# Optimization experiments

Measured on AMD Instinct MI355X. Metric: run time of the kernel, lower is better.

The kernel has to match this reference:

```python
import jax, jax.numpy as jnp
import numpy as np

N_NODES, N_EDGES, F_IN = 8192, 32768, 16
N_SUB, N_GRAPH = 512, 32
EDGE_DIM, HID = 5, 128
DIMS = [(16, 32), (32, 64), (64, 64)]  # (M_in, M_out) per NNConv layer


def _segment_mean(x, seg, n):
    s = jax.ops.segment_sum(x, seg, num_segments=n)
    c = jax.ops.segment_sum(jnp.ones((x.shape[0], 1), x.dtype), seg, num_segments=n)
    return s / jnp.maximum(c, 1.0)


def _nnconv(x, src, dst, eattr, W1, b1, W2, b2, root, bias):
    # edge MLP -> per-edge weight matrix theta: [E, M_in, M_out]
    h = jax.nn.relu(eattr @ W1 + b1)
    theta = (h @ W2 + b2).reshape(-1, x.shape[1], root.shape[1])
    msg = jnp.einsum('ei,eio->eo', x[src], theta)          # gather + per-edge matvec
    agg = jax.ops.segment_sum(msg, dst, num_segments=x.shape[0])  # scatter-add (aggr='add')
    return agg + x @ root + bias


def setup_inputs() -> dict:
    key = jax.random.key(0)
    ks = jax.random.split(key, 32)
    inp = {}
    inp['x'] = jax.random.normal(ks[0], (N_NODES, F_IN), jnp.float32)
    inp['edge_index'] = jax.random.randint(ks[1], (2, N_EDGES), 0, N_NODES)
    inp['edge_attr'] = jax.random.uniform(ks[2], (N_EDGES, EDGE_DIM), jnp.float32)
    inp['node_to_subgraph'] = jnp.sort(jax.random.randint(ks[3], (N_NODES,), 0, N_SUB))
    inp['subgraph_to_graph'] = jnp.sort(jax.random.randint(ks[4], (N_SUB,), 0, N_GRAPH))
    i = 5
    for l, (ci, co) in enumerate(DIMS):
        inp[f'W1_{l}'] = jax.random.normal(ks[i], (EDGE_DIM, HID), jnp.float32) * 0.1
        inp[f'b1_{l}'] = jnp.zeros((HID,), jnp.float32)
        inp[f'W2_{l}'] = jax.random.normal(ks[i + 1], (HID, ci * co), jnp.float32) * 0.05
        inp[f'b2_{l}'] = jnp.zeros((ci * co,), jnp.float32)
        inp[f'root_{l}'] = jax.random.normal(ks[i + 2], (ci, co), jnp.float32) * 0.1
        inp[f'bias_{l}'] = jnp.zeros((co,), jnp.float32)
        i += 3
    inp['fc1_w'] = jax.random.normal(ks[i], (64, 32), jnp.float32) * 0.1
    inp['fc1_b'] = jnp.zeros((32,), jnp.float32)
    inp['fc2_w'] = jax.random.normal(ks[i + 1], (32, 16), jnp.float32) * 0.1
    inp['fc2_b'] = jnp.zeros((16,), jnp.float32)
    inp['fc3_w'] = jax.random.normal(ks[i + 2], (16, 1), jnp.float32) * 0.1
    inp['fc3_b'] = jnp.zeros((1,), jnp.float32)
    return inp


def reference(x, edge_index, edge_attr, node_to_subgraph, subgraph_to_graph,
              W1_0, b1_0, W2_0, b2_0, root_0, bias_0,
              W1_1, b1_1, W2_1, b2_1, root_1, bias_1,
              W1_2, b1_2, W2_2, b2_2, root_2, bias_2,
              fc1_w, fc1_b, fc2_w, fc2_b, fc3_w, fc3_b):
    src, dst = edge_index[0], edge_index[1]
    layers = [(W1_0, b1_0, W2_0, b2_0, root_0, bias_0),
              (W1_1, b1_1, W2_1, b2_1, root_1, bias_1),
              (W1_2, b1_2, W2_2, b2_2, root_2, bias_2)]
    h = x
    for (W1, b1, W2, b2, root, bias) in layers:
        h = jax.nn.elu(_nnconv(h, src, dst, edge_attr, W1, b1, W2, b2, root, bias))
    h = _segment_mean(h, node_to_subgraph, N_SUB)      # global_mean_pool over subgraphs
    h = _segment_mean(h, subgraph_to_graph, N_GRAPH)   # global_mean_pool over graphs
    h = jax.nn.elu(h @ fc1_w + fc1_b)
    h = jax.nn.elu(h @ fc2_w + fc2_b)
    return (h @ fc3_w + fc3_b).reshape(-1)
```

## Files before the change

kernel.cpp:

```cpp
#include <hip/hip_runtime.h>

#define E_EDGES 32768
#define NN 8192
#define HID 128
#define KS 4

typedef _Float16 half8 __attribute__((ext_vector_type(8)));
typedef _Float16 half4 __attribute__((ext_vector_type(4)));
typedef float f32x4 __attribute__((ext_vector_type(4)));

__global__ void hist_k(const int* __restrict__ dst, int* __restrict__ hist) {
  int e = blockIdx.x * 256 + threadIdx.x;
  if (e < E_EDGES) atomicAdd(&hist[dst[e]], 1);
}

__global__ void scan_k(const int* __restrict__ hist, int* __restrict__ roff, int* __restrict__ cursor) {
  __shared__ int wsum[16];
  int t = threadIdx.x;
  int lane = t & 63, wv = t >> 6;
  int base = t * 8;
  int loc[8]; int s = 0;
#pragma unroll
  for (int j = 0; j < 8; ++j) { loc[j] = s; s += hist[base + j]; }
  int inc = s;
#pragma unroll
  for (int off = 1; off < 64; off <<= 1) {
    int u = __shfl_up(inc, off, 64);
    if (lane >= off) inc += u;
  }
  if (lane == 63) wsum[wv] = inc;
  __syncthreads();
  if (t < 64) {
    int u = (t < 16) ? wsum[t] : 0;
#pragma unroll
    for (int off = 1; off < 16; off <<= 1) {
      int x = __shfl_up(u, off, 64);
      if (lane >= off) u += x;
    }
    if (t < 16) wsum[t] = u;
  }
  __syncthreads();
  int excl = (wv ? wsum[wv - 1] : 0) + inc - s;
#pragma unroll
  for (int j = 0; j < 8; ++j) { int v = excl + loc[j]; roff[base + j] = v; cursor[base + j] = v; }
  if (t == 1023) roff[NN] = wsum[15];
}

__global__ void scatter_k(const int* __restrict__ dst, int* __restrict__ cursor, int* __restrict__ eidx) {
  int e = blockIdx.x * 256 + threadIdx.x;
  if (e < E_EDGES) { int p = atomicAdd(&cursor[dst[e]], 1); eidx[p] = e; }
}

template <int CI, int CO>
__device__ inline void prep8(int h8, const float* __restrict__ W2,
                             const float* __restrict__ b2, _Float16* __restrict__ out) {
  constexpr int Kmain = 128 * CI;
  constexpr int FC = CO / 16;
  int lane = h8 & 63;
  int quad = lane >> 4, l15 = lane & 15;
  int rest = h8 >> 6;
  int fc = rest & (FC - 1);
  int c = rest / FC;
  int k0 = c * 32 + quad * 8;
  int n = fc * 16 + l15;
  half8 r;
#pragma unroll
  for (int j = 0; j < 8; ++j) {
    int k = k0 + j;
    float v = 0.f;
    if (k < Kmain) v = W2[(size_t)k * CO + n];
    else if (k < Kmain + CI) v = b2[(k - Kmain) * CO + n];
    r[j] = (_Float16)v;
  }
  *(half8*)(out + (size_t)h8 * 8) = r;
}

__global__ void prep_zero_k(const float* __restrict__ W2_0, const float* __restrict__ b2_0, _Float16* __restrict__ o0,
                            const float* __restrict__ W2_1, const float* __restrict__ b2_1, _Float16* __restrict__ o1,
                            const float* __restrict__ W2_2, const float* __restrict__ b2_2, _Float16* __restrict__ o2,
                            int4* __restrict__ hist4, float4* __restrict__ pools4) {
  constexpr int H0 = 2176 * 32 / 8;
  constexpr int H1 = 4224 * 64 / 8;
  constexpr int H2 = 8320 * 64 / 8;
  constexpr int HT = H0 + H1 + H2;
  constexpr int ZH = NN / 4;
  constexpr int ZP = (512 * 64 + 512) / 4;
  int tid = blockIdx.x * 256 + threadIdx.x;
  if (tid < H0) prep8<16, 32>(tid, W2_0, b2_0, o0);
  else if (tid < H0 + H1) prep8<32, 64>(tid - H0, W2_1, b2_1, o1);
  else if (tid < HT) prep8<64, 64>(tid - H0 - H1, W2_2, b2_2, o2);
  else if (tid < HT + ZH) hist4[tid - HT] = int4{0, 0, 0, 0};
  else if (tid < HT + ZH + ZP) pools4[tid - HT - ZH] = float4{0.f, 0.f, 0.f, 0.f};
}

__device__ inline half8 pack8(float4 a, float4 b) {
  half8 r;
  r[0] = (_Float16)a.x; r[1] = (_Float16)a.y; r[2] = (_Float16)a.z; r[3] = (_Float16)a.w;
  r[4] = (_Float16)b.x; r[5] = (_Float16)b.y; r[6] = (_Float16)b.z; r[7] = (_Float16)b.w;
  return r;
}

__device__ __forceinline__ void gload_lds16(const _Float16* g, _Float16* l) {
  __builtin_amdgcn_global_load_lds(
      (__attribute__((address_space(1))) void*)(size_t)(const void*)g,
      (__attribute__((address_space(3))) void*)(size_t)(void*)l, 16, 0, 0);
}

template <int CI, int CO>
__launch_bounds__(256, 2)
__global__ void msg_mfma_k(const float* __restrict__ xcur, const int* __restrict__ src,
                           const int* __restrict__ eidx,
                           const float* __restrict__ eattr, const float* __restrict__ W1,
                           const float* __restrict__ b1, const _Float16* __restrict__ Bsw,
                           float* __restrict__ msgbuf) {
  constexpr int ME = 256;
  constexpr int HSTR = 36;
  constexpr int FC = CO / 16;
  constexpr int NMAIN = CI / 4;
  constexpr int XPN = (CI == 64) ? 2 : 1;
  constexpr int RHALF = 4 * FC * 64 * 8;

  __shared__ _Float16 he_s[ME * HSTR];
  __shared__ float ea_s[ME * 5];
  __shared__ float W1s[5 * 32];
  __shared__ float b1s[32];
  __shared__ int src_s[ME];
  __shared__ _Float16 bls[2 * RHALF];

  int t = threadIdx.x;
  int e0 = blockIdx.x * ME;
  int y = blockIdx.y;
  int hbeg = y * 32;

  {
    int eg = eidx[e0 + t];
    src_s[t] = src[eg];
#pragma unroll
    for (int d = 0; d < 5; ++d) ea_s[t * 5 + d] = eattr[eg * 5 + d];
  }
  if (t < 5 * 32) W1s[t] = W1[(t >> 5) * HID + hbeg + (t & 31)];
  if (t < 32) b1s[t] = b1[hbeg + t];
  __syncthreads();

  for (int j = t; j < 32 * ME; j += 256) {
    int hl = j & 31, e = j >> 5;
    float v = b1s[hl];
#pragma unroll
    for (int d = 0; d < 5; ++d) v += ea_s[e * 5 + d] * W1s[d * 32 + hl];
    he_s[e * HSTR + hl] = (_Float16)fmaxf(v, 0.f);
  }
  __syncthreads();

  int lane = t & 63;
  int w = t >> 6;
  int quad = lane >> 4, l15 = lane & 15;
  int qsh = (quad >> 1) << 4;
  int Rg0 = y * NMAIN;
  int NR = NMAIN + ((y == 3) ? 1 : 0);

  half8 xp[4][XPN];
  int hoff[4];
#pragma unroll
  for (int fr = 0; fr < 4; ++fr) {
    int e = w * 64 + fr * 16 + l15;
    const float* xr = xcur + (size_t)src_s[e] * CI;
    int i0 = (CI == 16) ? ((quad & 1) * 8) : (quad * 8);
    float4 v0 = *(const float4*)(xr + i0);
    float4 v1 = *(const float4*)(xr + i0 + 4);
    xp[fr][0] = pack8(v0, v1);
    if constexpr (CI == 64) {
      float4 v2 = *(const float4*)(xr + i0 + 32);
      float4 v3 = *(const float4*)(xr + i0 + 36);
      xp[fr][1] = pack8(v2, v3);
    }
    hoff[fr] = e * HSTR;
  }

  f32x4 acc[4][FC];
#pragma unroll
  for (int fr = 0; fr < 4; ++fr)
#pragma unroll
    for (int fc = 0; fc < FC; ++fc)
#pragma unroll
      for (int r = 0; r < 4; ++r) acc[fr][fc][r] = 0.f;

  auto stageR = [&](int rg, int buf) {
    const _Float16* gb = Bsw + (size_t)rg * RHALF + w * (FC * 512);
    _Float16* lb = bls + buf * RHALF + w * (FC * 512);
#pragma unroll
    for (int i = 0; i < FC; ++i)
      gload_lds16(gb + i * 512 + lane * 8, lb + i * 512);
  };

  stageR(Rg0, 0);
  stageR(Rg0 + 1, 1);

  for (int r = 0; r < NR; ++r) {
    if (r + 1 < NR) {
      if constexpr (FC == 4) asm volatile("s_waitcnt vmcnt(4)" ::: "memory");
      else                   asm volatile("s_waitcnt vmcnt(2)" ::: "memory");
    } else {
      asm volatile("s_waitcnt vmcnt(0)" ::: "memory");
    }
    __builtin_amdgcn_s_barrier();

    const _Float16* bp = bls + (r & 1) * RHALF;
    int c0 = (Rg0 + r) * 4;

    if (r < NMAIN) {
      unsigned int hp2[4];
      half4 hp4[4];
      if constexpr (CI == 64) {
        int oh = (c0 >> 1) - hbeg;
#pragma unroll
        for (int fr = 0; fr < 4; ++fr) hp2[fr] = *(const unsigned int*)(he_s + hoff[fr] + oh);
      } else if constexpr (CI == 32) {
        int oh = c0 - hbeg;
#pragma unroll
        for (int fr = 0; fr < 4; ++fr) hp4[fr] = *(const half4*)(he_s + hoff[fr] + oh);
      }
#pragma unroll
      for (int cr = 0; cr < 4; ++cr) {
        int c = c0 + cr;
        half8 a[4];
#pragma unroll
        for (int fr = 0; fr < 4; ++fr) {
          if constexpr (CI == 64) {
            unsigned short hb = (unsigned short)((cr >= 2) ? (hp2[fr] >> 16) : hp2[fr]);
            _Float16 hv = __builtin_bit_cast(_Float16, hb);
            a[fr] = xp[fr][cr & 1] * hv;
          } else if constexpr (CI == 32) {
            a[fr] = xp[fr][0] * hp4[fr][cr];
          } else {
            unsigned int hw = *(const unsigned int*)(he_s + hoff[fr] + (2 * c - hbeg));
            _Float16 hv = __builtin_bit_cast(_Float16, (unsigned short)(hw >> qsh));
            a[fr] = xp[fr][0] * hv;
          }
        }
#pragma unroll
        for (int fc = 0; fc < FC; ++fc) {
          half8 bf = *(const half8*)&bp[((cr * FC + fc) * 64 + lane) * 8];
#pragma unroll
          for (int fr = 0; fr < 4; ++fr)
            acc[fr][fc] = __builtin_amdgcn_mfma_f32_16x16x32_f16(a[fr], bf, acc[fr][fc], 0, 0, 0);
        }
      }
    } else {
#pragma unroll
      for (int cr = 0; cr < 4; ++cr) {
        half8 a[4];
#pragma unroll
        for (int fr = 0; fr < 4; ++fr) a[fr] = xp[fr][(CI == 64) ? (cr & 1) : 0];
#pragma unroll
        for (int fc = 0; fc < FC; ++fc) {
          half8 bf = *(const half8*)&bp[((cr * FC + fc) * 64 + lane) * 8];
#pragma unroll
          for (int fr = 0; fr < 4; ++fr)
            acc[fr][fc] = __builtin_amdgcn_mfma_f32_16x16x32_f16(a[fr], bf, acc[fr][fc], 0, 0, 0);
        }
      }
    }

    asm volatile("s_waitcnt lgkmcnt(0)" ::: "memory");
    __builtin_amdgcn_s_barrier();
    if (r + 2 < NR) stageR(Rg0 + r + 2, r & 1);
  }

#pragma unroll
  for (int fr = 0; fr < 4; ++fr)
#pragma unroll
    for (int fc = 0; fc < FC; ++fc)
#pragma unroll
      for (int r = 0; r < 4; ++r) {
        int el = w * 64 + fr * 16 + quad * 4 + r;
        int o = fc * 16 + l15;
        msgbuf[((size_t)(e0 + el) * KS + y) * CO + o] = acc[fr][fc][r];
      }
}

template <int CI, int CO, bool POOL>
__global__ void gather_elu_k(const float* __restrict__ xcur, const float* __restrict__ root,
                             const float* __restrict__ bias, const float* __restrict__ msgbuf,
                             const int* __restrict__ roff,
                             float* __restrict__ xnext, const int* __restrict__ n2s,
                             float* __restrict__ ssum, float* __restrict__ scnt) {
  constexpr int OV = CO / 4;
  constexpr int NB = 256 / OV;
  __shared__ float xs[NB * CI];
  int t = threadIdx.x;
  int n0 = blockIdx.x * NB;
  for (int j = t; j < NB * CI; j += 256) xs[j] = xcur[n0 * CI + j];
  __syncthreads();
  int nl = t / OV, o4 = t & (OV - 1);
  int n = n0 + nl;
  float4 a = ((const float4*)bias)[o4];
  const float4* root4 = (const float4*)root;
#pragma unroll
  for (int i = 0; i < CI; ++i) {
    float xv = xs[nl * CI + i];
    float4 rv = root4[i * OV + o4];
    a.x += xv * rv.x; a.y += xv * rv.y; a.z += xv * rv.z; a.w += xv * rv.w;
  }
  int j1 = roff[n + 1];
  const float4* mb4 = (const float4*)msgbuf;
  for (int p = roff[n]; p < j1; ++p) {
#pragma unroll
    for (int s = 0; s < KS; ++s) {
      float4 m = mb4[((size_t)p * KS + s) * OV + o4];
      a.x += m.x; a.y += m.y; a.z += m.z; a.w += m.w;
    }
  }
  float4 v;
  v.x = a.x > 0.f ? a.x : expm1f(a.x);
  v.y = a.y > 0.f ? a.y : expm1f(a.y);
  v.z = a.z > 0.f ? a.z : expm1f(a.z);
  v.w = a.w > 0.f ? a.w : expm1f(a.w);
  if constexpr (POOL) {
    int s = n2s[n];
    float* sb = &ssum[(s << 6) + o4 * 4];
    atomicAdd(sb + 0, v.x); atomicAdd(sb + 1, v.y);
    atomicAdd(sb + 2, v.z); atomicAdd(sb + 3, v.w);
    if (o4 == 0) atomicAdd(&scnt[s], 1.f);
  } else {
    ((float4*)xnext)[(size_t)n * OV + o4] = v;
  }
}

__global__ void pg_head_k(const float* __restrict__ ssum, const float* __restrict__ scnt,
                          const int* __restrict__ s2g,
                          const float* __restrict__ w1, const float* __restrict__ b1,
                          const float* __restrict__ w2, const float* __restrict__ b2,
                          const float* __restrict__ w3, const float* __restrict__ b3,
                          float* __restrict__ out) {
  int g = blockIdx.x;
  int t = threadIdx.x;
  __shared__ int s2s[512];
  __shared__ float hm[64], h1[32], h2[16];
  for (int i = t; i < 512; i += 64) s2s[i] = s2g[i];
  __syncthreads();
  float acc = 0.f, cnt = 0.f;
  for (int s = 0; s < 512; ++s) {
    if (s2s[s] == g) {
      acc += ssum[(s << 6) + t] / fmaxf(scnt[s], 1.f);
      cnt += 1.f;
    }
  }
  hm[t] = acc / fmaxf(cnt, 1.f);
  __syncthreads();
  if (t < 32) {
    float a = b1[t];
    for (int i = 0; i < 64; ++i) a += hm[i] * w1[i * 32 + t];
    h1[t] = a > 0.f ? a : expm1f(a);
  }
  __syncthreads();
  if (t < 16) {
    float a = b2[t];
    for (int i = 0; i < 32; ++i) a += h1[i] * w2[i * 16 + t];
    h2[t] = a > 0.f ? a : expm1f(a);
  }
  __syncthreads();
  if (t == 0) {
    float a = b3[0];
    for (int i = 0; i < 16; ++i) a += h2[i] * w3[i];
    out[g] = a;
  }
}

extern "C" void kernel_launch(void* const* d_in, const int* in_sizes, int n_in,
                              void* d_out, int out_size, void* d_ws, size_t ws_size,
                              hipStream_t stream) {
  (void)in_sizes; (void)n_in; (void)out_size; (void)ws_size;
  const float* x0 = (const float*)d_in[0];
  const int* ei = (const int*)d_in[1];
  const float* ea = (const float*)d_in[2];
  const int* n2s = (const int*)d_in[3];
  const int* s2g = (const int*)d_in[4];
  const float* W1_[3] = {(const float*)d_in[5], (const float*)d_in[11], (const float*)d_in[17]};
  const float* b1_[3] = {(const float*)d_in[6], (const float*)d_in[12], (const float*)d_in[18]};
  const float* W2_[3] = {(const float*)d_in[7], (const float*)d_in[13], (const float*)d_in[19]};
  const float* b2_[3] = {(const float*)d_in[8], (const float*)d_in[14], (const float*)d_in[20]};
  const float* rt_[3] = {(const float*)d_in[9], (const float*)d_in[15], (const float*)d_in[21]};
  const float* bs_[3] = {(const float*)d_in[10], (const float*)d_in[16], (const float*)d_in[22]};
  const float* fc1w = (const float*)d_in[23]; const float* fc1b = (const float*)d_in[24];
  const float* fc2w = (const float*)d_in[25]; const float* fc2b = (const float*)d_in[26];
  const float* fc3w = (const float*)d_in[27]; const float* fc3b = (const float*)d_in[28];
  float* out = (float*)d_out;

  const int* srcp = ei;
  const int* dstp = ei + E_EDGES;

  char* wsb = (char*)d_ws;
  size_t off = 0;
  auto alloc = [&](size_t bytes) {
    void* p = wsb + off;
    off += (bytes + 255) & ~(size_t)255;
    return p;
  };
  _Float16* Bsw0 = (_Float16*)alloc((size_t)2176 * 32 * 2);
  _Float16* Bsw1 = (_Float16*)alloc((size_t)4224 * 64 * 2);
  _Float16* Bsw2 = (_Float16*)alloc((size_t)8320 * 64 * 2);
  float* msgbuf = (float*)alloc((size_t)KS * E_EDGES * 64 * 4);
  float* x1 = (float*)alloc((size_t)NN * 32 * 4);
  float* x2 = (float*)alloc((size_t)NN * 64 * 4);
  int* hist = (int*)alloc((size_t)NN * 4);
  int* roff = (int*)alloc((size_t)(NN + 1) * 4);
  int* cursor = (int*)alloc((size_t)NN * 4);
  int* eidx = (int*)alloc((size_t)E_EDGES * 4);
  const int npool = 512 * 64 + 512;
  float* pools = (float*)alloc((size_t)npool * 4);
  float* ssum = pools;
  float* scnt = pools + 512 * 64;

  const int nprep = 109056 + 2048 + 8320;
  prep_zero_k<<<(nprep + 255) / 256, 256, 0, stream>>>(
      W2_[0], b2_[0], Bsw0, W2_[1], b2_[1], Bsw1, W2_[2], b2_[2], Bsw2,
      (int4*)hist, (float4*)pools);
  hist_k<<<E_EDGES / 256, 256, 0, stream>>>(dstp, hist);
  scan_k<<<1, 1024, 0, stream>>>(hist, roff, cursor);
  scatter_k<<<E_EDGES / 256, 256, 0, stream>>>(dstp, cursor, eidx);

  dim3 mg(E_EDGES / 256, KS);
  msg_mfma_k<16, 32><<<mg, 256, 0, stream>>>(x0, srcp, eidx, ea, W1_[0], b1_[0], Bsw0, msgbuf);
  gather_elu_k<16, 32, false><<<NN / 32, 256, 0, stream>>>(x0, rt_[0], bs_[0], msgbuf, roff, x1, nullptr, nullptr, nullptr);
  msg_mfma_k<32, 64><<<mg, 256, 0, stream>>>(x1, srcp, eidx, ea, W1_[1], b1_[1], Bsw1, msgbuf);
  gather_elu_k<32, 64, false><<<NN / 16, 256, 0, stream>>>(x1, rt_[1], bs_[1], msgbuf, roff, x2, nullptr, nullptr, nullptr);
  msg_mfma_k<64, 64><<<mg, 256, 0, stream>>>(x2, srcp, eidx, ea, W1_[2], b1_[2], Bsw2, msgbuf);
  gather_elu_k<64, 64, true><<<NN / 16, 256, 0, stream>>>(x2, rt_[2], bs_[2], msgbuf, roff, nullptr, n2s, ssum, scnt);

  pg_head_k<<<32, 64, 0, stream>>>(ssum, scnt, s2g, fc1w, fc1b, fc2w, fc2b, fc3w, fc3b, out);
}
```

Baseline: 278.6 us.

## Halve edge tile and split message-kernel warps across output columns and edges

The per-edge message MFMA kernel now processes 128 edges per block instead of 256, which doubles the grid. Its four warps are split between output-column fragments and edge groups instead of each warp covering 64 edges across all output columns. This gives each warp fewer accumulators and one B fragment load per row step, aiming at better occupancy and more blocks to fill the GPU. In exchange, each block stages the weight tiles for half as many edges, and source features are gathered redundantly by warps that share edges.

```diff
diff --git a/kernel.cpp b/kernel.cpp
--- a/kernel.cpp
+++ b/kernel.cpp
@@ -113,9 +113,12 @@
                            const float* __restrict__ eattr, const float* __restrict__ W1,
                            const float* __restrict__ b1, const _Float16* __restrict__ Bsw,
                            float* __restrict__ msgbuf) {
-  constexpr int ME = 256;
+  constexpr int ME = 128;
   constexpr int HSTR = 36;
   constexpr int FC = CO / 16;
+  constexpr int WN = (FC == 4) ? 4 : 2;
+  constexpr int WE = 4 / WN;
+  constexpr int FR = (ME / 16) / WE;
   constexpr int NMAIN = CI / 4;
   constexpr int XPN = (CI == 64) ? 2 : 1;
   constexpr int RHALF = 4 * FC * 64 * 8;
@@ -132,7 +135,7 @@
   int y = blockIdx.y;
   int hbeg = y * 32;
 
-  {
+  if (t < ME) {
     int eg = eidx[e0 + t];
     src_s[t] = src[eg];
 #pragma unroll
@@ -153,16 +156,17 @@
 
   int lane = t & 63;
   int w = t >> 6;
+  int wn = w % WN, we = w / WN;
   int quad = lane >> 4, l15 = lane & 15;
   int qsh = (quad >> 1) << 4;
   int Rg0 = y * NMAIN;
   int NR = NMAIN + ((y == 3) ? 1 : 0);
 
-  half8 xp[4][XPN];
-  int hoff[4];
-#pragma unroll
-  for (int fr = 0; fr < 4; ++fr) {
-    int e = w * 64 + fr * 16 + l15;
+  half8 xp[FR][XPN];
+  int hoff[FR];
+#pragma unroll
+  for (int fr = 0; fr < FR; ++fr) {
+    int e = we * (FR * 16) + fr * 16 + l15;
     const float* xr = xcur + (size_t)src_s[e] * CI;
     int i0 = (CI == 16) ? ((quad & 1) * 8) : (quad * 8);
     float4 v0 = *(const float4*)(xr + i0);
@@ -176,13 +180,11 @@
     hoff[fr] = e * HSTR;
   }
 
-  f32x4 acc[4][FC];
-#pragma unroll
-  for (int fr = 0; fr < 4; ++fr)
-#pragma unroll
-    for (int fc = 0; fc < FC; ++fc)
-#pragma unroll
-      for (int r = 0; r < 4; ++r) acc[fr][fc][r] = 0.f;
+  f32x4 acc[FR];
+#pragma unroll
+  for (int fr = 0; fr < FR; ++fr)
+#pragma unroll
+    for (int r = 0; r < 4; ++r) acc[fr][r] = 0.f;
 
   auto stageR = [&](int rg, int buf) {
     const _Float16* gb = Bsw + (size_t)rg * RHALF + w * (FC * 512);
@@ -208,55 +210,46 @@
     int c0 = (Rg0 + r) * 4;
 
     if (r < NMAIN) {
-      unsigned int hp2[4];
-      half4 hp4[4];
+      unsigned int hp2[FR];
+      half4 hp4[FR];
       if constexpr (CI == 64) {
         int oh = (c0 >> 1) - hbeg;
 #pragma unroll
-        for (int fr = 0; fr < 4; ++fr) hp2[fr] = *(const unsigned int*)(he_s + hoff[fr] + oh);
+        for (int fr = 0; fr < FR; ++fr) hp2[fr] = *(const unsigned int*)(he_s + hoff[fr] + oh);
       } else if constexpr (CI == 32) {
         int oh = c0 - hbeg;
 #pragma unroll
-        for (int fr = 0; fr < 4; ++fr) hp4[fr] = *(const half4*)(he_s + hoff[fr] + oh);
+        for (int fr = 0; fr < FR; ++fr) hp4[fr] = *(const half4*)(he_s + hoff[fr] + oh);
       }
 #pragma unroll
       for (int cr = 0; cr < 4; ++cr) {
         int c = c0 + cr;
-        half8 a[4];
-#pragma unroll
-        for (int fr = 0; fr < 4; ++fr) {
+        half8 bf = *(const half8*)&bp[((cr * FC + wn) * 64 + lane) * 8];
+#pragma unroll
+        for (int fr = 0; fr < FR; ++fr) {
+          half8 a;
           if constexpr (CI == 64) {
             unsigned short hb = (unsigned short)((cr >= 2) ? (hp2[fr] >> 16) : hp2[fr]);
             _Float16 hv = __builtin_bit_cast(_Float16, hb);
-            a[fr] = xp[fr][cr & 1] * hv;
+            a = xp[fr][cr & 1] * hv;
           } else if constexpr (CI == 32) {
-            a[fr] = xp[fr][0] * hp4[fr][cr];
+            a = xp[fr][0] * hp4[fr][cr];
           } else {
             unsigned int hw = *(const unsigned int*)(he_s + hoff[fr] + (2 * c - hbeg));
             _Float16 hv = __builtin_bit_cast(_Float16, (unsigned short)(hw >> qsh));
-            a[fr] = xp[fr][0] * hv;
+            a = xp[fr][0] * hv;
           }
-        }
-#pragma unroll
-        for (int fc = 0; fc < FC; ++fc) {
-          half8 bf = *(const half8*)&bp[((cr * FC + fc) * 64 + lane) * 8];
-#pragma unroll
-          for (int fr = 0; fr < 4; ++fr)
-            acc[fr][fc] = __builtin_amdgcn_mfma_f32_16x16x32_f16(a[fr], bf, acc[fr][fc], 0, 0, 0);
+          acc[fr] = __builtin_amdgcn_mfma_f32_16x16x32_f16(a, bf, acc[fr], 0, 0, 0);
         }
       }
     } else {
 #pragma unroll
       for (int cr = 0; cr < 4; ++cr) {
-        half8 a[4];
-#pragma unroll
-        for (int fr = 0; fr < 4; ++fr) a[fr] = xp[fr][(CI == 64) ? (cr & 1) : 0];
-#pragma unroll
-        for (int fc = 0; fc < FC; ++fc) {
-          half8 bf = *(const half8*)&bp[((cr * FC + fc) * 64 + lane) * 8];
-#pragma unroll
-          for (int fr = 0; fr < 4; ++fr)
-            acc[fr][fc] = __builtin_amdgcn_mfma_f32_16x16x32_f16(a[fr], bf, acc[fr][fc], 0, 0, 0);
+        half8 bf = *(const half8*)&bp[((cr * FC + wn) * 64 + lane) * 8];
+#pragma unroll
+        for (int fr = 0; fr < FR; ++fr) {
+          half8 a = xp[fr][(CI == 64) ? (cr & 1) : 0];
+          acc[fr] = __builtin_amdgcn_mfma_f32_16x16x32_f16(a, bf, acc[fr], 0, 0, 0);
         }
       }
     }
@@ -267,15 +260,13 @@
   }
 
 #pragma unroll
-  for (int fr = 0; fr < 4; ++fr)
-#pragma unroll
-    for (int fc = 0; fc < FC; ++fc)
-#pragma unroll
-      for (int r = 0; r < 4; ++r) {
-        int el = w * 64 + fr * 16 + quad * 4 + r;
-        int o = fc * 16 + l15;
-        msgbuf[((size_t)(e0 + el) * KS + y) * CO + o] = acc[fr][fc][r];
-      }
+  for (int fr = 0; fr < FR; ++fr)
+#pragma unroll
+    for (int r = 0; r < 4; ++r) {
+      int el = we * (FR * 16) + fr * 16 + quad * 4 + r;
+      int o = wn * 16 + l15;
+      msgbuf[((size_t)(e0 + el) * KS + y) * CO + o] = acc[fr][r];
+    }
 }
 
 template <int CI, int CO, bool POOL>
@@ -419,7 +410,7 @@
   scan_k<<<1, 1024, 0, stream>>>(hist, roff, cursor);
   scatter_k<<<E_EDGES / 256, 256, 0, stream>>>(dstp, cursor, eidx);
 
-  dim3 mg(E_EDGES / 256, KS);
+  dim3 mg(E_EDGES / 128, KS);
   msg_mfma_k<16, 32><<<mg, 256, 0, stream>>>(x0, srcp, eidx, ea, W1_[0], b1_[0], Bsw0, msgbuf);
   gather_elu_k<16, 32, false><<<NN / 32, 256, 0, stream>>>(x0, rt_[0], bs_[0], msgbuf, roff, x1, nullptr, nullptr, nullptr);
   msg_mfma_k<32, 64><<<mg, 256, 0, stream>>>(x1, srcp, eidx, ea, W1_[1], b1_[1], Bsw1, msgbuf);
```

Measured after the change: 300.1 us. 1.08x slower.
